# Kernel optimization log

Measured on AMD Instinct MI355X. Metric: run time of the kernel, lower is better.

## Reference

```python
import jax, jax.numpy as jnp
import numpy as np

N = 100000   # nodes
E = 400000   # edges (before self-loops)
G = 4000     # graphs in batch
F_IN = 32    # node_embedding
HID = 128    # hidden_channels
H = 3        # heads (hard-coded in module)
W3 = H * HID # 384, post-concat width
NC = 10      # num_classes
NL = 4       # num_layers
NEG_SLOPE = 0.2


def _lin(key, fan_in, fan_out):
    return jax.random.normal(key, (fan_in, fan_out), jnp.float32) * (1.0 / np.sqrt(fan_in))


def setup_inputs() -> dict:
    key = jax.random.key(0)
    ks = iter(jax.random.split(key, 40))
    x = jax.random.normal(next(ks), (N, F_IN), jnp.float32)
    edge_index = jax.random.randint(next(ks), (2, E), 0, N, dtype=jnp.int32)
    batch = jnp.sort(jax.random.randint(next(ks), (N,), 0, G, dtype=jnp.int32))
    inp = dict(x=x, edge_index=edge_index, batch=batch)
    # MLP stem
    inp['lin1_w'] = _lin(next(ks), F_IN, 2 * HID); inp['lin1_b'] = jnp.zeros((2 * HID,), jnp.float32)
    inp['lin2_w'] = _lin(next(ks), 2 * HID, HID);  inp['lin2_b'] = jnp.zeros((HID,), jnp.float32)
    # conv1: GATConv(HID -> HID, heads=3)
    inp['w0'] = _lin(next(ks), HID, W3)
    inp['as0'] = jax.random.normal(next(ks), (H, HID), jnp.float32) * 0.1
    inp['ad0'] = jax.random.normal(next(ks), (H, HID), jnp.float32) * 0.1
    inp['b0'] = jnp.zeros((W3,), jnp.float32)
    # remaining NL-1 convs: GATConv(W3 -> HID, heads=3), stacked
    inp['wl'] = jnp.stack([_lin(next(ks), W3, W3) for _ in range(NL - 1)])
    inp['asl'] = jax.random.normal(next(ks), (NL - 1, H, HID), jnp.float32) * 0.1
    inp['adl'] = jax.random.normal(next(ks), (NL - 1, H, HID), jnp.float32) * 0.1
    inp['bl'] = jnp.zeros((NL - 1, W3), jnp.float32)
    # batch norms (NL total, all width W3)
    inp['gamma'] = jnp.ones((NL, W3), jnp.float32)
    inp['beta'] = jnp.zeros((NL, W3), jnp.float32)
    # head
    inp['lin3_w'] = _lin(next(ks), W3, HID); inp['lin3_b'] = jnp.zeros((HID,), jnp.float32)
    inp['lin4_w'] = _lin(next(ks), HID, NC); inp['lin4_b'] = jnp.zeros((NC,), jnp.float32)
    return inp


def _gat(x, W, a_src, a_dst, bias, src, dst):
    # PyG GATConv, concat heads. x: [N, Fin]
    h = (x @ W).reshape(N, H, HID)                       # [N, H, C]
    es = jnp.einsum('nhc,hc->nh', h, a_src)              # [N, H]
    ed = jnp.einsum('nhc,hc->nh', h, a_dst)
    e = jax.nn.leaky_relu(es[src] + ed[dst], NEG_SLOPE)  # [Etot, H]
    m = jax.ops.segment_max(e, dst, num_segments=N)      # segment softmax over incoming edges
    p = jnp.exp(e - m[dst])
    s = jax.ops.segment_sum(p, dst, num_segments=N)
    alpha = p / s[dst]                                   # every node has a self-loop -> s>0
    out = jax.ops.segment_sum(alpha[:, :, None] * h[src], dst, num_segments=N)
    return out.reshape(N, W3) + bias


def _bn(x, g, b):
    mu = x.mean(0)
    var = x.var(0)
    return (x - mu) * jax.lax.rsqrt(var + 1e-5) * g + b


def reference(x, edge_index, batch, lin1_w, lin1_b, lin2_w, lin2_b,
              w0, as0, ad0, b0, wl, asl, adl, bl, gamma, beta,
              lin3_w, lin3_b, lin4_w, lin4_b):
    loop = jnp.arange(N, dtype=edge_index.dtype)
    src = jnp.concatenate([edge_index[0], loop])  # add_self_loops=True (PyG default)
    dst = jnp.concatenate([edge_index[1], loop])
    h = jax.nn.relu(x @ lin1_w + lin1_b)
    h = jax.nn.relu(h @ lin2_w + lin2_b)
    h = _gat(h, w0, as0, ad0, b0, src, dst)
    h = _bn(h, gamma[0], beta[0])
    for i in range(NL - 1):
        h = _gat(h, wl[i], asl[i], adl[i], bl[i], src, dst)
        h = _bn(h, gamma[i + 1], beta[i + 1])
    # global mean pool over graphs
    sums = jax.ops.segment_sum(h, batch, num_segments=G)
    cnt = jax.ops.segment_sum(jnp.ones((N,), h.dtype), batch, num_segments=G)
    g = sums / jnp.maximum(cnt, 1.0)[:, None]
    g = jax.nn.relu(g @ lin3_w + lin3_b)
    logits = g @ lin4_w + lin4_b
    return jax.nn.log_softmax(logits, axis=-1)
```

## Files before the change

### kernel.cpp

```cpp
#include <hip/hip_runtime.h>

#define NN      100000
#define NN2     100096
#define NE      400000
#define ETOT    500000
#define NG      4000
#define W3D     384
#define HIDD    128
#define NCLS    10
#define NSLICE  256

typedef unsigned short u16;
typedef unsigned int   u32;
typedef unsigned long long u64;
typedef __attribute__((ext_vector_type(8))) short short8;
typedef __attribute__((ext_vector_type(4))) float f32x4;

static __device__ __forceinline__ float bf2f(u16 u) {
  return __uint_as_float(((u32)u) << 16);
}
static __device__ __forceinline__ float bflo(u32 u) {
  return __uint_as_float(u << 16);
}
static __device__ __forceinline__ float bfhi(u32 u) {
  return __uint_as_float(u & 0xffff0000u);
}
static __device__ __forceinline__ u16 f2b(float f) {
  u32 u = __float_as_uint(f);
  u32 r = (u + 0x7fffu + ((u >> 16) & 1u)) >> 16;
  return (u16)r;
}

static __device__ __forceinline__ void llds16(const u16* g, u16* l) {
  __builtin_amdgcn_global_load_lds(
      (const __attribute__((address_space(1))) void*)(u64)(const void*)g,
      (__attribute__((address_space(3))) void*)(u64)(void*)l, 16, 0, 0);
}

#define WAITV0() asm volatile("s_waitcnt vmcnt(0)" ::: "memory")

__global__ void mg_zero_out(float* out, int n) {
  int i = blockIdx.x * 256 + threadIdx.x;
  if (i < n) out[i] = 0.f;
}

__global__ void mg_cvt_x(const float* __restrict__ x, u16* __restrict__ Xb) {
  int idx = blockIdx.x * 256 + threadIdx.x;
  if (idx >= NN2 * 64) return;
  int row = idx >> 6, col = idx & 63;
  Xb[idx] = (row < NN && col < 32) ? f2b(x[row * 32 + col]) : (u16)0;
}

__global__ void mg_transpose_pad(const float* __restrict__ in, u16* __restrict__ out,
                                 int K, int Nn, int Kpad) {
  int idx = blockIdx.x * 256 + threadIdx.x;
  if (idx >= Nn * Kpad) return;
  int n = idx / Kpad, kp = idx - n * Kpad;
  out[idx] = (kp < K) ? f2b(in[kp * Nn + n]) : (u16)0;
}

__global__ void mg_fold_w(const u16* __restrict__ Wt, const float* __restrict__ scale,
                          const float* __restrict__ shift, u16* __restrict__ Wp,
                          float* __restrict__ bp) {
  __shared__ float red[128];
  int j = blockIdx.x, t = threadIdx.x;
  const u16* src = Wt + (size_t)j * (W3D + 8);
  u16* dst = Wp + (size_t)j * (W3D + 8);
  float acc = 0.f;
  for (int kp = t; kp < W3D + 8; kp += 128) {
    int kt = (kp < W3D) ? kp : 0;
    float w = bf2f(src[kp]);
    dst[kp] = f2b(w * scale[kt]);
    acc += w * shift[kt];
  }
  red[t] = acc; __syncthreads();
  for (int off = 64; off; off >>= 1) {
    if (t < off) red[t] += red[t + off];
    __syncthreads();
  }
  if (t == 0) bp[j] = red[0];
}

__global__ void mg_edge_histo(const int* __restrict__ ei, int* __restrict__ deg) {
  int e = blockIdx.x * 256 + threadIdx.x;
  if (e >= ETOT) return;
  int d = (e < NE) ? ei[NE + e] : (e - NE);
  atomicAdd(&deg[d], 1);
}

__global__ void mg_scan1(const int* __restrict__ in, int* __restrict__ bsum, int n) {
  __shared__ int sd[256];
  int tid = threadIdx.x;
  int base = blockIdx.x * 1024 + tid * 4;
  int s = 0;
#pragma unroll
  for (int j = 0; j < 4; ++j) { int i = base + j; if (i < n) s += in[i]; }
  sd[tid] = s; __syncthreads();
  for (int off = 128; off > 0; off >>= 1) {
    if (tid < off) sd[tid] += sd[tid + off];
    __syncthreads();
  }
  if (tid == 0) bsum[blockIdx.x] = sd[0];
}

__global__ void mg_scan2(int* __restrict__ bsum, int nb) {
  __shared__ int sd[256];
  int tid = threadIdx.x;
  int v = (tid < nb) ? bsum[tid] : 0;
  sd[tid] = v; __syncthreads();
  for (int off = 1; off < 256; off <<= 1) {
    int t = (tid >= off) ? sd[tid - off] : 0;
    __syncthreads();
    sd[tid] += t;
    __syncthreads();
  }
  if (tid < nb) bsum[tid] = sd[tid] - v;
}

__global__ void mg_scan3(const int* __restrict__ in, const int* __restrict__ bexcl,
                         int* __restrict__ out, int n) {
  __shared__ int sd[256];
  int tid = threadIdx.x;
  int base = blockIdx.x * 1024 + tid * 4;
  int loc[4]; int s = 0;
#pragma unroll
  for (int j = 0; j < 4; ++j) { int i = base + j; loc[j] = (i < n) ? in[i] : 0; s += loc[j]; }
  sd[tid] = s; __syncthreads();
  for (int off = 1; off < 256; off <<= 1) {
    int t = (tid >= off) ? sd[tid - off] : 0;
    __syncthreads();
    sd[tid] += t;
    __syncthreads();
  }
  int run = sd[tid] - s + bexcl[blockIdx.x];
#pragma unroll
  for (int j = 0; j < 4; ++j) {
    int i = base + j;
    if (i < n) { out[i] = run; run += loc[j]; if (i == n - 1) out[n] = run; }
  }
}

__global__ void mg_edge_scatter(const int* __restrict__ ei, int* __restrict__ fill,
                                int* __restrict__ colsrc) {
  int e = blockIdx.x * 256 + threadIdx.x;
  if (e >= ETOT) return;
  int s, d;
  if (e < NE) { s = ei[e]; d = ei[NE + e]; } else { s = e - NE; d = s; }
  int pos = atomicAdd(&fill[d], 1);
  colsrc[pos] = s;
}

__global__ void mg_graph_ptr(const int* __restrict__ batch, int* __restrict__ gptr) {
  int g = blockIdx.x * 256 + threadIdx.x;
  if (g > NG) return;
  if (g == NG) { gptr[NG] = NN; return; }
  int lo = 0, hi = NN;
  while (lo < hi) { int mid = (lo + hi) >> 1; if (batch[mid] < g) lo = mid + 1; else hi = mid; }
  gptr[g] = lo;
}

#define CP 136

template<int K>
__global__ __launch_bounds__(512, 2) void mg_gemm(
    const u16* __restrict__ Ag, const u16* __restrict__ Bt,
    int MT, int Mstore, int Nn,
    u16* __restrict__ Cb, const float* __restrict__ bias, int relu,
    const float* __restrict__ asrc, const float* __restrict__ adst,
    float* __restrict__ aes, float* __restrict__ aed) {
  constexpr int KP = K + 8;
  constexpr int NITER = K / 32;
  constexpr int CSZ = (K == 384) ? 3 : ((K >= 128) ? 2 : 1);
  constexpr int CH = NITER / CSZ;
  static_assert(CH * CSZ == NITER && (CH & 1) == 0, "chunking");
  __shared__ u16 lds[128 * KP + 8 * 16 * CP];
  u16* Blds = lds;
  int tid = threadIdx.x;
  int lane = tid & 63, wv = tid >> 6;
  int nidx = blockIdx.y, n0 = nidx * 128;
  int lr = lane & 15, lq = lane >> 4;

  {
    const u16* Bg = Bt + (size_t)n0 * KP;
    constexpr int BBYTES = 128 * KP * 2;
    constexpr int FULL = BBYTES / 8192;
    constexpr int REMC = (BBYTES - FULL * 8192) / 16;
#pragma unroll
    for (int s = 0; s < FULL; ++s) {
      int off = s * 4096 + wv * 512 + lane * 8;
      llds16(Bg + off, Blds + off);
    }
    if (REMC > 0 && wv * 64 + lane < REMC) {
      int off = FULL * 4096 + wv * 512 + lane * 8;
      llds16(Bg + off, Blds + off);
    }
  }

  float bvv[8];
#pragma unroll
  for (int ni = 0; ni < 8; ++ni)
    bvv[ni] = bias ? bias[n0 + ni * 16 + lr] : 0.f;

  WAITV0();
  __syncthreads();

  u16* strip = lds + 128 * KP + wv * (16 * CP);

  int t0 = (int)(((long long)blockIdx.x * MT) / gridDim.x);
  int t1 = (int)(((long long)(blockIdx.x + 1) * MT) / gridDim.x);

  f32x4 acc[2][8];
  short8 bufE[2][CSZ], bufO[2][CSZ];

  auto loadCh = [&](short8 (&buf)[2][CSZ], int t, int ch) {
    const u16* Ar = Ag + (size_t)(t * 256 + wv * 32 + lr) * K + lq * 8 + ch * (CSZ * 32);
#pragma unroll
    for (int mi = 0; mi < 2; ++mi)
#pragma unroll
      for (int s = 0; s < CSZ; ++s)
        buf[mi][s] = *(const short8*)(Ar + (size_t)mi * 16 * K + s * 32);
  };
  auto compCh = [&](short8 (&buf)[2][CSZ], int ch) {
#pragma unroll
    for (int s = 0; s < CSZ; ++s) {
      int it = ch * CSZ + s;
      short8 bfr[8];
#pragma unroll
      for (int ni = 0; ni < 8; ++ni)
        bfr[ni] = *(const short8*)(Blds + (ni * 16 + lr) * KP + it * 32 + lq * 8);
#pragma unroll
      for (int mi = 0; mi < 2; ++mi)
#pragma unroll
        for (int ni = 0; ni < 8; ++ni)
          acc[mi][ni] = __builtin_amdgcn_mfma_f32_16x16x32_bf16(buf[mi][s], bfr[ni], acc[mi][ni], 0, 0, 0);
    }
  };

  loadCh(bufE, t0, 0);

  for (int t = t0; t < t1; ++t) {
    int rowbase = t * 256 + wv * 32;
#pragma unroll
    for (int mi = 0; mi < 2; ++mi)
#pragma unroll
      for (int ni = 0; ni < 8; ++ni) acc[mi][ni] = (f32x4){0.f, 0.f, 0.f, 0.f};

#pragma unroll
    for (int ch = 0; ch < CH; ch += 2) {
      loadCh(bufO, t, ch + 1);
      compCh(bufE, ch);
      if (ch + 2 < CH) loadCh(bufE, t, ch + 2);
      else if (t + 1 < t1) loadCh(bufE, t + 1, 0);
      compCh(bufO, ch + 1);
    }

#pragma unroll
    for (int mi = 0; mi < 2; ++mi) {
#pragma unroll
      for (int ni = 0; ni < 8; ++ni) {
#pragma unroll
        for (int r = 0; r < 4; ++r) {
          float v = acc[mi][ni][r] + bvv[ni];
          if (relu) v = fmaxf(v, 0.f);
          strip[(lq * 4 + r) * CP + ni * 16 + lr] = f2b(v);
        }
      }
      int row16 = lane >> 2, cb = lane & 3;
      const u16* src = strip + row16 * CP + cb * 32;
      uint4 c0 = *(const uint4*)(src);
      uint4 c1 = *(const uint4*)(src + 8);
      uint4 c2 = *(const uint4*)(src + 16);
      uint4 c3 = *(const uint4*)(src + 24);
      int mrow = rowbase + mi * 16 + row16;
      u16* gout = Cb + (size_t)mrow * Nn + n0 + cb * 32;
      *(uint4*)(gout)      = c0;
      *(uint4*)(gout + 8)  = c1;
      *(uint4*)(gout + 16) = c2;
      *(uint4*)(gout + 24) = c3;

      if (aes) {
        const float* ap = asrc + n0 + cb * 32;
        const float* dp = adst + n0 + cb * 32;
        float se = 0.f, de = 0.f;
        uint4 cj[4] = {c0, c1, c2, c3};
#pragma unroll
        for (int j = 0; j < 4; ++j) {
          float4 A0 = *(const float4*)(ap + j * 8);
          float4 A1 = *(const float4*)(ap + j * 8 + 4);
          float4 D0 = *(const float4*)(dp + j * 8);
          float4 D1 = *(const float4*)(dp + j * 8 + 4);
          uint4 rv = cj[j];
          float v0 = bflo(rv.x), v1 = bfhi(rv.x), v2 = bflo(rv.y), v3 = bfhi(rv.y);
          float v4 = bflo(rv.z), v5 = bfhi(rv.z), v6 = bflo(rv.w), v7 = bfhi(rv.w);
          se += v0 * A0.x + v1 * A0.y + v2 * A0.z + v3 * A0.w
              + v4 * A1.x + v5 * A1.y + v6 * A1.z + v7 * A1.w;
          de += v0 * D0.x + v1 * D0.y + v2 * D0.z + v3 * D0.w
              + v4 * D1.x + v5 * D1.y + v6 * D1.z + v7 * D1.w;
        }
        se += __shfl_xor(se, 1); se += __shfl_xor(se, 2);
        de += __shfl_xor(de, 1); de += __shfl_xor(de, 2);
        if (cb == 0 && mrow < Mstore) {
          aes[mrow * 4 + nidx] = se;
          aed[mrow * 4 + nidx] = de;
        }
      }
    }
  }
}

__global__ __launch_bounds__(256) void mg_aggregate(
    const u16* __restrict__ B, const float* __restrict__ es,
    const float* __restrict__ ed, const int* __restrict__ rowptr,
    const int* __restrict__ colsrc, const float* __restrict__ bias,
    u16* __restrict__ A, float* __restrict__ stats) {
  __shared__ float bS[4 * W3D];
  __shared__ float bQ[4 * W3D];
  int wv = threadIdx.x >> 6, lane = threadIdx.x & 63;
  if (lane < 48) {
    int h = lane >> 4;
    int cc = lane * 8;
    float4 bv0 = *(const float4*)(bias + cc);
    float4 bv1 = *(const float4*)(bias + cc + 4);
    float stS[8], stQ[8];
#pragma unroll
    for (int j = 0; j < 8; ++j) { stS[j] = 0.f; stQ[j] = 0.f; }
#pragma unroll
    for (int sub = 0; sub < 2; ++sub) {
      int n = blockIdx.x * 8 + wv * 2 + sub;
      int r0 = rowptr[n], r1 = rowptr[n + 1];
      float4 edv = *(const float4*)(ed + 4 * n);
      float4 esn = *(const float4*)(es + 4 * n);
      float s0 = esn.x + edv.x; s0 = (s0 > 0.f) ? s0 : 0.2f * s0;
      float s1 = esn.y + edv.y; s1 = (s1 > 0.f) ? s1 : 0.2f * s1;
      float s2 = esn.z + edv.z; s2 = (s2 > 0.f) ? s2 : 0.2f * s2;
      float mh  = (h == 0) ? s0 : ((h == 1) ? s1 : s2);
      float edh = (h == 0) ? edv.x : ((h == 1) ? edv.y : edv.z);
      float accv[8];
#pragma unroll
      for (int j = 0; j < 8; ++j) accv[j] = 0.f;
      float ssum = 0.f;
      int sA = __builtin_amdgcn_readfirstlane(colsrc[r0]);
      float4 evA = *(const float4*)(es + 4 * sA);
      uint4  rvA = *(const uint4*)(B + (size_t)sA * W3D + cc);
      float4 evB = evA; uint4 rvB = rvA;
      if (r0 + 1 < r1) {
        int sB = __builtin_amdgcn_readfirstlane(colsrc[r0 + 1]);
        evB = *(const float4*)(es + 4 * sB);
        rvB = *(const uint4*)(B + (size_t)sB * W3D + cc);
      }
      for (int r = r0; r < r1; ++r) {
        float4 ev = evA; uint4 rv = rvA;
        evA = evB; rvA = rvB;
        if (r + 2 < r1) {
          int sC = __builtin_amdgcn_readfirstlane(colsrc[r + 2]);
          evB = *(const float4*)(es + 4 * sC);
          rvB = *(const uint4*)(B + (size_t)sC * W3D + cc);
        }
        float e = ((h == 0) ? ev.x : ((h == 1) ? ev.y : ev.z)) + edh;
        e = (e > 0.f) ? e : 0.2f * e;
        float p = __expf(e - mh);
        ssum += p;
        accv[0] += p * bflo(rv.x); accv[1] += p * bfhi(rv.x);
        accv[2] += p * bflo(rv.y); accv[3] += p * bfhi(rv.y);
        accv[4] += p * bflo(rv.z); accv[5] += p * bfhi(rv.z);
        accv[6] += p * bflo(rv.w); accv[7] += p * bfhi(rv.w);
      }
      float inv = 1.0f / ssum;
      float v[8];
      v[0] = accv[0] * inv + bv0.x; v[1] = accv[1] * inv + bv0.y;
      v[2] = accv[2] * inv + bv0.z; v[3] = accv[3] * inv + bv0.w;
      v[4] = accv[4] * inv + bv1.x; v[5] = accv[5] * inv + bv1.y;
      v[6] = accv[6] * inv + bv1.z; v[7] = accv[7] * inv + bv1.w;
      uint4 st;
      st.x = (u32)f2b(v[0]) | ((u32)f2b(v[1]) << 16);
      st.y = (u32)f2b(v[2]) | ((u32)f2b(v[3]) << 16);
      st.z = (u32)f2b(v[4]) | ((u32)f2b(v[5]) << 16);
      st.w = (u32)f2b(v[6]) | ((u32)f2b(v[7]) << 16);
      *(uint4*)(A + (size_t)n * W3D + cc) = st;
#pragma unroll
      for (int j = 0; j < 8; ++j) { stS[j] += v[j]; stQ[j] += v[j] * v[j]; }
    }
    *(float4*)(bS + wv * W3D + cc)     = (float4){stS[0], stS[1], stS[2], stS[3]};
    *(float4*)(bS + wv * W3D + cc + 4) = (float4){stS[4], stS[5], stS[6], stS[7]};
    *(float4*)(bQ + wv * W3D + cc)     = (float4){stQ[0], stQ[1], stQ[2], stQ[3]};
    *(float4*)(bQ + wv * W3D + cc + 4) = (float4){stQ[4], stQ[5], stQ[6], stQ[7]};
  }
  __syncthreads();
  for (int t = threadIdx.x; t < W3D; t += 256) {
    float s = 0.f, q = 0.f;
#pragma unroll
    for (int w = 0; w < 4; ++w) { s += bS[w * W3D + t]; q += bQ[w * W3D + t]; }
    float* sl = stats + (size_t)(blockIdx.x & (NSLICE - 1)) * 768;
    atomicAdd(&sl[t], s);
    atomicAdd(&sl[W3D + t], q);
  }
}

__global__ void mg_bn_finalize(const float* __restrict__ stats, const float* __restrict__ gamma,
                               const float* __restrict__ beta, float* __restrict__ scale,
                               float* __restrict__ shift) {
  int c = threadIdx.x;
  float s = 0.f, q = 0.f;
  for (int b = 0; b < NSLICE; ++b) { s += stats[b * 768 + c]; q += stats[b * 768 + W3D + c]; }
  const float invN = 1.0f / (float)NN;
  float mu = s * invN;
  float var = fmaxf(q * invN - mu * mu, 0.f);
  float inv = rsqrtf(var + 1e-5f);
  float g = gamma[c], be = beta[c];
  scale[c] = g * inv;
  shift[c] = be - mu * g * inv;
}

__global__ void mg_pool(const u16* __restrict__ A, const float* __restrict__ scale,
                        const float* __restrict__ shift, const int* __restrict__ gptr,
                        float* __restrict__ pooled) {
  int g = blockIdx.x, c = threadIdx.x;
  int r0 = gptr[g], r1 = gptr[g + 1];
  float acc = 0.f;
  for (int n = r0; n < r1; ++n) acc += bf2f(A[(size_t)n * W3D + c]);
  int cnt = r1 - r0;
  float v = (cnt > 0) ? (acc / (float)cnt) * scale[c] + shift[c] : 0.f;
  pooled[g * W3D + c] = v;
}

__global__ void mg_head(const float* __restrict__ pooled, const float* __restrict__ w3,
                        const float* __restrict__ b3, const float* __restrict__ w4,
                        const float* __restrict__ b4, float* __restrict__ out) {
  __shared__ float p[W3D];
  __shared__ float g2[HIDD];
  __shared__ float lg[NCLS];
  int g = blockIdx.x, t = threadIdx.x;
  for (int i = t; i < W3D; i += 128) p[i] = pooled[g * W3D + i];
  __syncthreads();
  float acc = 0.f;
  for (int k = 0; k < W3D; ++k) acc += p[k] * w3[k * HIDD + t];
  g2[t] = fmaxf(acc + b3[t], 0.f);
  __syncthreads();
  if (t < NCLS) {
    float a = 0.f;
    for (int k = 0; k < HIDD; ++k) a += g2[k] * w4[k * NCLS + t];
    lg[t] = a + b4[t];
  }
  __syncthreads();
  if (t < NCLS) {
    float m = -1e30f;
#pragma unroll
    for (int j = 0; j < NCLS; ++j) m = fmaxf(m, lg[j]);
    float se = 0.f;
#pragma unroll
    for (int j = 0; j < NCLS; ++j) se += __expf(lg[j] - m);
    out[g * NCLS + t] = lg[t] - m - __logf(se);
  }
}

extern "C" void kernel_launch(void* const* d_in, const int* in_sizes, int n_in,
                              void* d_out, int out_size, void* d_ws, size_t ws_size,
                              hipStream_t stream) {
  const float* x     = (const float*)d_in[0];
  const int*   ei    = (const int*)d_in[1];
  const int*   batch = (const int*)d_in[2];
  const float* w1    = (const float*)d_in[3];
  const float* b1    = (const float*)d_in[4];
  const float* w2    = (const float*)d_in[5];
  const float* b2    = (const float*)d_in[6];
  const float* w0    = (const float*)d_in[7];
  const float* as0   = (const float*)d_in[8];
  const float* ad0   = (const float*)d_in[9];
  const float* b0    = (const float*)d_in[10];
  const float* wl    = (const float*)d_in[11];
  const float* asl   = (const float*)d_in[12];
  const float* adl   = (const float*)d_in[13];
  const float* bl    = (const float*)d_in[14];
  const float* gamma = (const float*)d_in[15];
  const float* beta  = (const float*)d_in[16];
  const float* w3    = (const float*)d_in[17];
  const float* b3    = (const float*)d_in[18];
  const float* w4    = (const float*)d_in[19];
  const float* b4    = (const float*)d_in[20];
  float* out = (float*)d_out;

  char* w = (char*)d_ws;
  auto alloc = [&](size_t bytes) -> void* {
    void* p = (void*)w;
    w += (bytes + 255) & ~(size_t)255;
    return p;
  };
  u16*   P      = (u16*)alloc((size_t)NN2 * W3D * 2);
  u16*   Q      = (u16*)alloc((size_t)NN2 * W3D * 2);
  float* es     = (float*)alloc((size_t)NN * 4 * 4);
  float* ed     = (float*)alloc((size_t)NN * 4 * 4);
  int*   deg    = (int*)alloc((size_t)NN * 4);
  int*   rowptr = (int*)alloc((size_t)(NN + 1) * 4);
  int*   fill   = (int*)alloc((size_t)NN * 4);
  int*   colsrc = (int*)alloc((size_t)ETOT * 4);
  int*   bsum   = (int*)alloc(256 * 4);
  float* stats  = (float*)alloc((size_t)NSLICE * 768 * 4);
  float* scale  = (float*)alloc(W3D * 4);
  float* shift  = (float*)alloc(W3D * 4);
  float* bprime = (float*)alloc(W3D * 4);
  int*   gptr   = (int*)alloc((size_t)(NG + 1) * 4);
  float* pooled = (float*)alloc((size_t)NG * W3D * 4);
  u16*   W1T    = (u16*)alloc((size_t)256 * 72 * 2);
  u16*   W2T    = (u16*)alloc((size_t)128 * 264 * 2);
  u16*   W0T    = (u16*)alloc((size_t)384 * 136 * 2);
  u16*   WlT    = (u16*)alloc((size_t)3 * 384 * 392 * 2);
  u16*   WpT    = (u16*)alloc((size_t)384 * 392 * 2);
  u16*   Xb     = Q;

  if ((size_t)(w - (char*)d_ws) > ws_size) {
    mg_zero_out<<<(out_size + 255) / 256, 256, 0, stream>>>(out, out_size);
    return;
  }

  mg_cvt_x<<<(NN2 * 64 + 255) / 256, 256, 0, stream>>>(x, Xb);
  mg_transpose_pad<<<(256 * 72 + 255) / 256, 256, 0, stream>>>(w1, W1T, 32, 256, 72);
  mg_transpose_pad<<<(128 * 264 + 255) / 256, 256, 0, stream>>>(w2, W2T, 256, 128, 264);
  mg_transpose_pad<<<(384 * 136 + 255) / 256, 256, 0, stream>>>(w0, W0T, 128, 384, 136);
  for (int i = 0; i < 3; ++i)
    mg_transpose_pad<<<(384 * 392 + 255) / 256, 256, 0, stream>>>(
        wl + (size_t)i * 384 * 384, WlT + (size_t)i * 384 * 392, 384, 384, 392);

  hipMemsetAsync(deg, 0, (size_t)NN * 4, stream);
  mg_edge_histo<<<(ETOT + 255) / 256, 256, 0, stream>>>(ei, deg);
  int nb = (NN + 1023) / 1024;
  mg_scan1<<<nb, 256, 0, stream>>>(deg, bsum, NN);
  mg_scan2<<<1, 256, 0, stream>>>(bsum, nb);
  mg_scan3<<<nb, 256, 0, stream>>>(deg, bsum, rowptr, NN);
  hipMemcpyAsync(fill, rowptr, (size_t)NN * 4, hipMemcpyDeviceToDevice, stream);
  mg_edge_scatter<<<(ETOT + 255) / 256, 256, 0, stream>>>(ei, fill, colsrc);
  mg_graph_ptr<<<(NG + 1 + 255) / 256, 256, 0, stream>>>(batch, gptr);

  dim3 blk(512);
  const int MT = NN2 / 256;

  mg_gemm<64><<<dim3(128, 2), blk, 0, stream>>>(Xb, W1T, MT, NN, 256,
                                                P, b1, 1,
                                                nullptr, nullptr, nullptr, nullptr);
  mg_gemm<256><<<dim3(256, 1), blk, 0, stream>>>(P, W2T, MT, NN, 128,
                                                 Q, b2, 1,
                                                 nullptr, nullptr, nullptr, nullptr);

  for (int i = 0; i < 4; ++i) {
    const float* bi_g = nullptr;
    const u16* Bt;
    if (i == 0) {
      Bt = W0T;
    } else {
      mg_fold_w<<<384, 128, 0, stream>>>(WlT + (size_t)(i - 1) * 384 * 392,
                                         scale, shift, WpT, bprime);
      Bt = WpT;
      bi_g = bprime;
    }
    const float* as = (i == 0) ? as0 : (asl + (size_t)(i - 1) * 384);
    const float* ad = (i == 0) ? ad0 : (adl + (size_t)(i - 1) * 384);
    const float* bi = (i == 0) ? b0  : (bl  + (size_t)(i - 1) * 384);
    hipMemsetAsync(stats, 0, (size_t)NSLICE * 768 * 4, stream);
    if (i == 0)
      mg_gemm<128><<<dim3(85, 3), blk, 0, stream>>>(Q, Bt, MT, NN, W3D,
                                                    P, bi_g, 0,
                                                    as, ad, es, ed);
    else
      mg_gemm<384><<<dim3(85, 3), blk, 0, stream>>>(Q, Bt, MT, NN, W3D,
                                                    P, bi_g, 0,
                                                    as, ad, es, ed);
    mg_aggregate<<<NN / 8, 256, 0, stream>>>(P, es, ed, rowptr, colsrc, bi, Q, stats);
    mg_bn_finalize<<<1, 384, 0, stream>>>(stats, gamma + (size_t)i * W3D,
                                          beta + (size_t)i * W3D, scale, shift);
  }

  mg_pool<<<NG, 384, 0, stream>>>(Q, scale, shift, gptr, pooled);
  mg_head<<<NG, 128, 0, stream>>>(pooled, w3, b3, w4, b4, out);
}
```

Baseline: 1.054 ms.

## Precompute edge attention weights, deepen aggregate prefetch, remap GEMM blocks per XCD

A new per-edge kernel computes the exponentiated attention weights for all heads into a CSR-ordered array, using the self-loop logit as the softmax shift. The aggregation loop then reads precomputed weights and processes edges in groups of four with deeper index and row prefetching, which takes the exp and the extra gathers off its critical path. Separately, the GEMM remaps block IDs so that consecutive M-chunks land on the same XCD, which should improve L2 reuse. In exchange there is an extra kernel launch and per-layer writes and reads of a 500K×4 float buffer, plus a destination array filled at scatter time.

After: 972.0 us. 1.08x faster.

```diff
diff --git a/kernel.cpp b/kernel.cpp
--- a/kernel.cpp
+++ b/kernel.cpp
@@ -141,13 +141,14 @@
 }
 
 __global__ void mg_edge_scatter(const int* __restrict__ ei, int* __restrict__ fill,
-                                int* __restrict__ colsrc) {
+                                int* __restrict__ colsrc, int* __restrict__ dstc) {
   int e = blockIdx.x * 256 + threadIdx.x;
   if (e >= ETOT) return;
   int s, d;
   if (e < NE) { s = ei[e]; d = ei[NE + e]; } else { s = e - NE; d = s; }
   int pos = atomicAdd(&fill[d], 1);
   colsrc[pos] = s;
+  dstc[pos] = d;
 }
 
 __global__ void mg_graph_ptr(const int* __restrict__ batch, int* __restrict__ gptr) {
@@ -157,6 +158,36 @@
   int lo = 0, hi = NN;
   while (lo < hi) { int mid = (lo + hi) >> 1; if (batch[mid] < g) lo = mid + 1; else hi = mid; }
   gptr[g] = lo;
+}
+
+__global__ __launch_bounds__(256) void mg_edge_p(
+    const int* __restrict__ colsrc, const int* __restrict__ dstc,
+    const float* __restrict__ es, const float* __restrict__ ed,
+    float* __restrict__ pcsr) {
+  int e = blockIdx.x * 256 + threadIdx.x;
+  if (e >= ETOT) return;
+  int s = colsrc[e], d = dstc[e];
+  float4 a = *(const float4*)(es + 4 * s);
+  float4 sd = *(const float4*)(es + 4 * d);
+  float4 dd = *(const float4*)(ed + 4 * d);
+  float4 p;
+  {
+    float ev = a.x + dd.x; ev = (ev > 0.f) ? ev : 0.2f * ev;
+    float mv = sd.x + dd.x; mv = (mv > 0.f) ? mv : 0.2f * mv;
+    p.x = __expf(ev - mv);
+  }
+  {
+    float ev = a.y + dd.y; ev = (ev > 0.f) ? ev : 0.2f * ev;
+    float mv = sd.y + dd.y; mv = (mv > 0.f) ? mv : 0.2f * mv;
+    p.y = __expf(ev - mv);
+  }
+  {
+    float ev = a.z + dd.z; ev = (ev > 0.f) ? ev : 0.2f * ev;
+    float mv = sd.z + dd.z; mv = (mv > 0.f) ? mv : 0.2f * mv;
+    p.z = __expf(ev - mv);
+  }
+  p.w = 0.f;
+  *(float4*)(pcsr + (size_t)e * 4) = p;
 }
 
 #define CP 136
@@ -177,7 +208,18 @@
   u16* Blds = lds;
   int tid = threadIdx.x;
   int lane = tid & 63, wv = tid >> 6;
-  int nidx = blockIdx.y, n0 = nidx * 128;
+
+  int gx = gridDim.x, gy = gridDim.y;
+  int nwg = gx * gy;
+  int lin = (int)blockIdx.y * gx + blockIdx.x;
+  int q = nwg >> 3, r8 = nwg & 7;
+  int xcd = lin & 7, sidx = lin >> 3;
+  int nlin = (xcd < r8) ? (xcd * (q + 1) + sidx)
+                        : (r8 * (q + 1) + (xcd - r8) * q + sidx);
+  int mchunk = nlin / gy;
+  int nidx = nlin - mchunk * gy;
+  int n0 = nidx * 128;
+
   int lr = lane & 15, lq = lane >> 4;
 
   {
@@ -206,8 +248,8 @@
 
   u16* strip = lds + 128 * KP + wv * (16 * CP);
 
-  int t0 = (int)(((long long)blockIdx.x * MT) / gridDim.x);
-  int t1 = (int)(((long long)(blockIdx.x + 1) * MT) / gridDim.x);
+  int t0 = (int)(((long long)mchunk * MT) / gx);
+  int t1 = (int)(((long long)(mchunk + 1) * MT) / gx);
 
   f32x4 acc[2][8];
   short8 bufE[2][CSZ], bufO[2][CSZ];
@@ -309,9 +351,9 @@
 }
 
 __global__ __launch_bounds__(256) void mg_aggregate(
-    const u16* __restrict__ B, const float* __restrict__ es,
-    const float* __restrict__ ed, const int* __restrict__ rowptr,
-    const int* __restrict__ colsrc, const float* __restrict__ bias,
+    const u16* __restrict__ B, const float* __restrict__ pcsr,
+    const int* __restrict__ rowptr, const int* __restrict__ colsrc,
+    const float* __restrict__ bias,
     u16* __restrict__ A, float* __restrict__ stats) {
   __shared__ float bS[4 * W3D];
   __shared__ float bQ[4 * W3D];
@@ -328,43 +370,45 @@
     for (int sub = 0; sub < 2; ++sub) {
       int n = blockIdx.x * 8 + wv * 2 + sub;
       int r0 = rowptr[n], r1 = rowptr[n + 1];
-      float4 edv = *(const float4*)(ed + 4 * n);
-      float4 esn = *(const float4*)(es + 4 * n);
-      float s0 = esn.x + edv.x; s0 = (s0 > 0.f) ? s0 : 0.2f * s0;
-      float s1 = esn.y + edv.y; s1 = (s1 > 0.f) ? s1 : 0.2f * s1;
-      float s2 = esn.z + edv.z; s2 = (s2 > 0.f) ? s2 : 0.2f * s2;
-      float mh  = (h == 0) ? s0 : ((h == 1) ? s1 : s2);
-      float edh = (h == 0) ? edv.x : ((h == 1) ? edv.y : edv.z);
       float accv[8];
 #pragma unroll
       for (int j = 0; j < 8; ++j) accv[j] = 0.f;
       float ssum = 0.f;
-      int sA = __builtin_amdgcn_readfirstlane(colsrc[r0]);
-      float4 evA = *(const float4*)(es + 4 * sA);
-      uint4  rvA = *(const uint4*)(B + (size_t)sA * W3D + cc);
-      float4 evB = evA; uint4 rvB = rvA;
-      if (r0 + 1 < r1) {
-        int sB = __builtin_amdgcn_readfirstlane(colsrc[r0 + 1]);
-        evB = *(const float4*)(es + 4 * sB);
-        rvB = *(const uint4*)(B + (size_t)sB * W3D + cc);
+
+      int   c0, c1, c2, c3, cb0, cb1, cb2, cb3;
+      float p0, p1, p2, p3, pb0, pb1, pb2, pb3;
+      uint4 v0, v1, v2, v3;
+
+#define IDX_(CV, PV, RR) { int _i = ((RR) < r1) ? (RR) : (r1 - 1);          \
+      CV = colsrc[_i]; PV = pcsr[(size_t)_i * 4 + h]; }
+#define BLD_(VV, CV) { int _s = __builtin_amdgcn_readfirstlane(CV);         \
+      VV = *(const uint4*)(B + (size_t)_s * W3D + cc); }
+#define CMP_(PV, VV, RR) { float _pv = ((RR) < r1) ? PV : 0.f;              \
+      ssum += _pv;                                                          \
+      accv[0] += _pv * bflo(VV.x); accv[1] += _pv * bfhi(VV.x);             \
+      accv[2] += _pv * bflo(VV.y); accv[3] += _pv * bfhi(VV.y);             \
+      accv[4] += _pv * bflo(VV.z); accv[5] += _pv * bfhi(VV.z);             \
+      accv[6] += _pv * bflo(VV.w); accv[7] += _pv * bfhi(VV.w); }
+
+      IDX_(c0,  p0,  r0 + 0) IDX_(c1,  p1,  r0 + 1)
+      IDX_(c2,  p2,  r0 + 2) IDX_(c3,  p3,  r0 + 3)
+      IDX_(cb0, pb0, r0 + 4) IDX_(cb1, pb1, r0 + 5)
+      IDX_(cb2, pb2, r0 + 6) IDX_(cb3, pb3, r0 + 7)
+      BLD_(v0, c0) BLD_(v1, c1) BLD_(v2, c2) BLD_(v3, c3)
+
+      for (int base = r0; base < r1; base += 4) {
+        CMP_(p0, v0, base + 0)  BLD_(v0, cb0)
+        CMP_(p1, v1, base + 1)  BLD_(v1, cb1)
+        CMP_(p2, v2, base + 2)  BLD_(v2, cb2)
+        CMP_(p3, v3, base + 3)  BLD_(v3, cb3)
+        p0 = pb0; p1 = pb1; p2 = pb2; p3 = pb3;
+        IDX_(cb0, pb0, base + 8)  IDX_(cb1, pb1, base + 9)
+        IDX_(cb2, pb2, base + 10) IDX_(cb3, pb3, base + 11)
       }
-      for (int r = r0; r < r1; ++r) {
-        float4 ev = evA; uint4 rv = rvA;
-        evA = evB; rvA = rvB;
-        if (r + 2 < r1) {
-          int sC = __builtin_amdgcn_readfirstlane(colsrc[r + 2]);
-          evB = *(const float4*)(es + 4 * sC);
-          rvB = *(const uint4*)(B + (size_t)sC * W3D + cc);
-        }
-        float e = ((h == 0) ? ev.x : ((h == 1) ? ev.y : ev.z)) + edh;
-        e = (e > 0.f) ? e : 0.2f * e;
-        float p = __expf(e - mh);
-        ssum += p;
-        accv[0] += p * bflo(rv.x); accv[1] += p * bfhi(rv.x);
-        accv[2] += p * bflo(rv.y); accv[3] += p * bfhi(rv.y);
-        accv[4] += p * bflo(rv.z); accv[5] += p * bfhi(rv.z);
-        accv[6] += p * bflo(rv.w); accv[7] += p * bfhi(rv.w);
-      }
+#undef IDX_
+#undef BLD_
+#undef CMP_
+
       float inv = 1.0f / ssum;
       float v[8];
       v[0] = accv[0] * inv + bv0.x; v[1] = accv[1] * inv + bv0.y;
@@ -493,6 +537,8 @@
   int*   rowptr = (int*)alloc((size_t)(NN + 1) * 4);
   int*   fill   = (int*)alloc((size_t)NN * 4);
   int*   colsrc = (int*)alloc((size_t)ETOT * 4);
+  int*   dstc   = (int*)alloc((size_t)ETOT * 4);
+  float* pcsr   = (float*)alloc((size_t)ETOT * 4 * 4);
   int*   bsum   = (int*)alloc(256 * 4);
   float* stats  = (float*)alloc((size_t)NSLICE * 768 * 4);
   float* scale  = (float*)alloc(W3D * 4);
@@ -527,11 +573,12 @@
   mg_scan2<<<1, 256, 0, stream>>>(bsum, nb);
   mg_scan3<<<nb, 256, 0, stream>>>(deg, bsum, rowptr, NN);
   hipMemcpyAsync(fill, rowptr, (size_t)NN * 4, hipMemcpyDeviceToDevice, stream);
-  mg_edge_scatter<<<(ETOT + 255) / 256, 256, 0, stream>>>(ei, fill, colsrc);
+  mg_edge_scatter<<<(ETOT + 255) / 256, 256, 0, stream>>>(ei, fill, colsrc, dstc);
   mg_graph_ptr<<<(NG + 1 + 255) / 256, 256, 0, stream>>>(batch, gptr);
 
   dim3 blk(512);
   const int MT = NN2 / 256;
+  const int EPB = (ETOT + 255) / 256;
 
   mg_gemm<64><<<dim3(128, 2), blk, 0, stream>>>(Xb, W1T, MT, NN, 256,
                                                 P, b1, 1,
@@ -563,7 +610,8 @@
       mg_gemm<384><<<dim3(85, 3), blk, 0, stream>>>(Q, Bt, MT, NN, W3D,
                                                     P, bi_g, 0,
                                                     as, ad, es, ed);
-    mg_aggregate<<<NN / 8, 256, 0, stream>>>(P, es, ed, rowptr, colsrc, bi, Q, stats);
+    mg_edge_p<<<EPB, 256, 0, stream>>>(colsrc, dstc, es, ed, pcsr);
+    mg_aggregate<<<NN / 8, 256, 0, stream>>>(P, pcsr, rowptr, colsrc, bi, Q, stats);
     mg_bn_finalize<<<1, 384, 0, stream>>>(stats, gamma + (size_t)i * W3D,
                                           beta + (size_t)i * W3D, scale, shift);
   }
```
